# Optimization experiments

Hardware: AMD Instinct MI355X
Metric: run time of the kernel (lower is better)

The kernel has to match this reference:

```python
import jax, jax.numpy as jnp
import numpy as np

N_NODES = 100000
N_EDGES = 1600000
F_IN = 128
HID = 64
N_CLS = 40


def _sage_conv(x, src, dst, Wl, bl, Wr, num_nodes):
    # PyG SAGEConv (aggr='mean', root_weight=True, normalize=False):
    # out = lin_l(mean_{j in N(i)} x_j) + lin_r(x_i)
    msg = x[src]                                              # [E, F] gather
    agg = jax.ops.segment_sum(msg, dst, num_segments=num_nodes)
    deg = jax.ops.segment_sum(jnp.ones_like(dst, dtype=x.dtype), dst,
                              num_segments=num_nodes)
    mean = agg / jnp.maximum(deg, 1.0)[:, None]               # [N, F]
    return mean @ Wl.T + bl + x @ Wr.T


def setup_inputs() -> dict:
    key = jax.random.key(0)
    ks = jax.random.split(key, 16)

    def lin(k, out_d, in_d):
        bound = 1.0 / np.sqrt(in_d)
        return jax.random.uniform(k, (out_d, in_d), jnp.float32, -bound, bound)

    x = jax.random.normal(ks[0], (N_NODES, F_IN), jnp.float32)
    edge_index = jax.random.randint(ks[1], (2, N_EDGES), 0, N_NODES, jnp.int64)

    return {
        "x": x,
        "edge_index": edge_index,
        "W1l": lin(ks[2], HID, F_IN), "b1": jnp.zeros((HID,), jnp.float32),
        "W1r": lin(ks[3], HID, F_IN),
        "W2l": lin(ks[4], HID, HID), "b2": jnp.zeros((HID,), jnp.float32),
        "W2r": lin(ks[5], HID, HID),
        "W3l": lin(ks[6], HID, HID), "b3": jnp.zeros((HID,), jnp.float32),
        "W3r": lin(ks[7], HID, HID),
        "Wout": lin(ks[8], N_CLS, HID),
        "bout": jnp.zeros((N_CLS,), jnp.float32),
    }


def reference(x, edge_index, W1l, b1, W1r, W2l, b2, W2r, W3l, b3, W3r, Wout, bout):
    src, dst = edge_index[0], edge_index[1]
    n = x.shape[0]
    h = _sage_conv(x, src, dst, W1l, b1, W1r, n)
    h = jax.nn.elu(h)
    h = _sage_conv(h, src, dst, W2l, b2, W2r, n)
    h = jax.nn.elu(h)
    h = _sage_conv(h, src, dst, W3l, b3, W3r, n)
    return h @ Wout.T + bout
```

## Files before the change

### kernel.cpp

```cpp
#include <hip/hip_runtime.h>


static inline size_t ws_align(size_t x) { return (x + 511) & ~size_t(511); }

#define MAXBC  104
#define CAPL   96
#define EB_CAP 24576

using frag_ab = __attribute__((ext_vector_type(8))) short;
using f32x4   = __attribute__((ext_vector_type(4))) float;
using us4     = __attribute__((ext_vector_type(4))) unsigned short;

__device__ inline short f2bf(float f) {
    unsigned u = __builtin_bit_cast(unsigned, f);
    u += 0x7fff + ((u >> 16) & 1);
    return (short)(u >> 16);
}
__device__ inline float b2f(unsigned short h) {
    unsigned u = ((unsigned)h) << 16;
    return __builtin_bit_cast(float, u);
}


__global__ void zero_kernel(int* __restrict__ p, int n) {
    int i = blockIdx.x * blockDim.x + threadIdx.x;
    if (i < n) p[i] = 0;
}

__global__ void prep_all(const float* __restrict__ W1l, const float* __restrict__ W1r,
                         const float* __restrict__ W2l, const float* __restrict__ W2r,
                         const float* __restrict__ W3l, const float* __restrict__ W3r,
                         unsigned short* __restrict__ fw) {
    const int idx = blockIdx.x * 256 + threadIdx.x;
    if (idx >= 32768) return;
    const float* W;
    unsigned short* out;
    int F, rel;
    if (idx < 8192)       { W = W1l; out = fw;        F = 128; rel = idx; }
    else if (idx < 16384) { W = W1r; out = fw + 8192; F = 128; rel = idx - 8192; }
    else {
        const int q = (idx - 16384) >> 12;
        rel = (idx - 16384) & 4095;
        F = 64;
        W = (q == 0) ? W2l : (q == 1) ? W2r : (q == 2) ? W3l : W3r;
        out = fw + 16384 + q * 4096;
    }
    const int k = rel % F;
    const int col = rel / F;
    out[(k >> 3) * 512 + col * 8 + (k & 7)] = (unsigned short)f2bf(W[rel]);
}


__global__ void pass1_bin(const int* __restrict__ src, const int* __restrict__ dst,
                          int* __restrict__ bcur, unsigned* __restrict__ ebuf,
                          int nE, int nN, int nbc) {
    __shared__ unsigned lbuf[MAXBC][CAPL];
    __shared__ int bcnt[MAXBC];
    __shared__ int gbase[MAXBC];
    const int t = threadIdx.x;
    const int e0 = blockIdx.x * 4096;
    for (int i = t; i < MAXBC; i += 256) bcnt[i] = 0;
    __syncthreads();
#pragma unroll
    for (int q = 0; q < 16; ++q) {
        const int e = e0 + q * 256 + t;
        if (e < nE) {
            const unsigned d = (unsigned)dst[e];
            const unsigned s = (unsigned)src[e];
            if (d < (unsigned)nN && s < (unsigned)nN) {
                const int cb = (int)(d >> 10);
                const unsigned v = ((d & 1023u) << 17) | s;
                const int pos = atomicAdd(&bcnt[cb], 1);
                if (pos < CAPL) {
                    lbuf[cb][pos] = v;
                } else {
                    const int gp = atomicAdd(&bcur[cb], 1);
                    if (gp < EB_CAP) ebuf[(size_t)cb * EB_CAP + gp] = v;
                }
            }
        }
    }
    __syncthreads();
    for (int b = t; b < nbc; b += 256) {
        const int cnt = min(bcnt[b], CAPL);
        bcnt[b] = cnt;
        gbase[b] = (cnt > 0) ? atomicAdd(&bcur[b], cnt) : 0;
    }
    __syncthreads();
    const int wid = t >> 6, lane = t & 63;
    for (int b = wid; b < nbc; b += 4) {
        const int cnt = bcnt[b];
        const int gb = gbase[b];
        for (int i = lane; i < cnt; i += 64) {
            const int gp = gb + i;
            if (gp < EB_CAP) ebuf[(size_t)b * EB_CAP + gp] = lbuf[b][i];
        }
    }
}

__global__ void scan_buckets(const int* __restrict__ bcur, int* __restrict__ bbase, int nbc) {
    __shared__ int sdata[256];
    const int t = threadIdx.x;
    const int v = (t < nbc) ? min(bcur[t], EB_CAP) : 0;
    sdata[t] = v;
    __syncthreads();
    for (int off = 1; off < 256; off <<= 1) {
        int add = (t >= off) ? sdata[t - off] : 0;
        __syncthreads();
        sdata[t] += add;
        __syncthreads();
    }
    if (t < nbc) bbase[t] = sdata[t] - v;
}

__global__ void pass2_build(const unsigned* __restrict__ ebuf,
                            const int* __restrict__ bcur, const int* __restrict__ bbase,
                            int* __restrict__ rowptr, int* __restrict__ csr,
                            int nN, int nbc) {
    __shared__ int lcnt[1024];
    __shared__ int lcur[1024];
    __shared__ int sdata[256];
    const int b = blockIdx.x;
    const int node0 = b << 10;
    const int nloc = min(1024, nN - node0);
    if (nloc <= 0) return;
    const int cnt  = min(bcur[b], EB_CAP);
    const int base = bbase[b];
    const int t = threadIdx.x;
    const unsigned* eb = ebuf + (size_t)b * EB_CAP;

    for (int i = t; i < 1024; i += 256) lcnt[i] = 0;
    __syncthreads();
    for (int i = t; i < cnt; i += 256) atomicAdd(&lcnt[eb[i] >> 17], 1);
    __syncthreads();
    int v[4];
    int tsum = 0;
#pragma unroll
    for (int q = 0; q < 4; ++q) { v[q] = lcnt[t * 4 + q]; tsum += v[q]; }
    sdata[t] = tsum;
    __syncthreads();
    for (int off = 1; off < 256; off <<= 1) {
        int add = (t >= off) ? sdata[t - off] : 0;
        __syncthreads();
        sdata[t] += add;
        __syncthreads();
    }
    int run = sdata[t] - tsum;
#pragma unroll
    for (int q = 0; q < 4; ++q) {
        const int l = t * 4 + q;
        lcur[l] = run;
        if (l < nloc) rowptr[node0 + l] = base + run;
        run += v[q];
    }
    if (b == nbc - 1 && t == 0) rowptr[nN] = base + cnt;
    __syncthreads();
    for (int i = t; i < cnt; i += 256) {
        const unsigned ev = eb[i];
        const int pos = atomicAdd(&lcur[ev >> 17], 1);
        csr[base + pos] = (int)((ev & 0x1FFFFu) << 7);
    }
}

template<int F, bool AF32>
__global__ void proj2_mfma(const void* __restrict__ Aptr,
                           const unsigned short* __restrict__ fwl,
                           const unsigned short* __restrict__ fwr,
                           const float* __restrict__ bias,
                           unsigned short* __restrict__ xl,
                           float* __restrict__ xr,
                           int nN) {
    const int t    = threadIdx.x;
    const int wave = t >> 6;
    const int lane = t & 63;
    const int lg   = lane >> 4;
    const int lr   = lane & 15;
    const int row0 = blockIdx.x * 64 + wave * 16;

    const float*          Af = (const float*)Aptr;
    const unsigned short* Ab = (const unsigned short*)Aptr;

    f32x4 accl[4] = {};
    f32x4 accr[4] = {};

#pragma unroll
    for (int ks = 0; ks < F / 32; ++ks) {
        const int k0 = ks * 32 + lg * 8;
        frag_ab afr;
        {
            int row = row0 + lr;
            if (row >= nN) row = nN - 1;
            if constexpr (AF32) {
                const float4 f0 = *reinterpret_cast<const float4*>(Af + (size_t)row * F + k0);
                const float4 f1 = *reinterpret_cast<const float4*>(Af + (size_t)row * F + k0 + 4);
                afr[0] = f2bf(f0.x); afr[1] = f2bf(f0.y); afr[2] = f2bf(f0.z); afr[3] = f2bf(f0.w);
                afr[4] = f2bf(f1.x); afr[5] = f2bf(f1.y); afr[6] = f2bf(f1.z); afr[7] = f2bf(f1.w);
            } else {
                afr = *reinterpret_cast<const frag_ab*>(Ab + (size_t)row * F + k0);
            }
        }
        const int ob = (ks * 4 + lg) * 512;
#pragma unroll
        for (int nf = 0; nf < 4; ++nf) {
            const int col = nf * 16 + lr;
            const frag_ab bl = *reinterpret_cast<const frag_ab*>(fwl + ob + col * 8);
            const frag_ab br = *reinterpret_cast<const frag_ab*>(fwr + ob + col * 8);
            accl[nf] = __builtin_amdgcn_mfma_f32_16x16x32_bf16(afr, bl, accl[nf], 0, 0, 0);
            accr[nf] = __builtin_amdgcn_mfma_f32_16x16x32_bf16(afr, br, accr[nf], 0, 0, 0);
        }
    }

#pragma unroll
    for (int nf = 0; nf < 4; ++nf) {
        const int col = nf * 16 + lr;
        const float bv = bias[col];
#pragma unroll
        for (int j = 0; j < 4; ++j) {
            const int row = row0 + lg * 4 + j;
            if (row < nN) {
                xl[(size_t)row * 64 + col] = (unsigned short)f2bf(accl[nf][j]);
                xr[(size_t)row * 64 + col] = accr[nf][j] + bv;
            }
        }
    }
}

template<bool DOELU>
__global__ void gather_kernel(const unsigned short* __restrict__ xl,
                              const float* __restrict__ xr,
                              const int* __restrict__ rowptr, const int* __restrict__ csr,
                              unsigned short* __restrict__ outp, int nN, int nE) {
    const int node = blockIdx.x * (blockDim.x >> 6) + (threadIdx.x >> 6);
    if (node >= nN) return;
    const int lane = threadIdx.x & 63;
    int b = rowptr[node];
    int e = rowptr[node + 1];
    b = max(0, min(b, nE));
    e = max(b, min(e, nE));
    b = __builtin_amdgcn_readfirstlane(b);
    e = __builtin_amdgcn_readfirstlane(e);
    const float d = (float)(e - b);
    const char* xlb = (const char*)xl + (lane << 1);

    float acc = 0.f;
    int i = b;
    for (; i + 16 <= e; i += 16) {
        unsigned short v[16];
#pragma unroll
        for (int j = 0; j < 16; ++j) {
            const unsigned s = (unsigned)csr[i + j];
            v[j] = *(const unsigned short*)(xlb + s);
        }
#pragma unroll
        for (int j = 0; j < 16; ++j) acc += b2f(v[j]);
    }
    if (i < e) {
        const int lim = e - i;
        unsigned short v[16];
#pragma unroll
        for (int j = 0; j < 16; ++j) {
            const unsigned s = (unsigned)csr[i + min(j, lim - 1)];
            v[j] = *(const unsigned short*)(xlb + s);
        }
#pragma unroll
        for (int j = 0; j < 16; ++j) acc += (j < lim) ? b2f(v[j]) : 0.f;
    }

    float vout = acc / fmaxf(d, 1.0f) + xr[(size_t)node * 64 + lane];
    if (DOELU) vout = vout > 0.f ? vout : expm1f(vout);
    outp[(size_t)node * 64 + lane] = (unsigned short)f2bf(vout);
}

template<int F, int NOUT>
__global__ void head_kernel(const unsigned short* __restrict__ A,
                            const float* __restrict__ W,
                            const float* __restrict__ bias,
                            float* __restrict__ out, int nN) {
    constexpr int NCH = F / 32;
    __shared__ float As[64][36];
    __shared__ float Bs[32][64];

    const int t = threadIdx.x;
    const int block0 = blockIdx.x * 64;
    const int tm = (t >> 4) << 2;
    const int tn = (t & 15) << 2;

    float acc[4][4] = {};

    for (int ch = 0; ch < NCH; ++ch) {
        const int kg0 = ch * 32;
        {
            const int kk = (t & 7) * 4;
#pragma unroll
            for (int r = 0; r < 2; ++r) {
                const int n = (t >> 3) + r * 32;
                const int node = block0 + n;
                float4 v = make_float4(0.f, 0.f, 0.f, 0.f);
                if (node < nN) {
                    const us4 u = *reinterpret_cast<const us4*>(A + (size_t)node * F + kg0 + kk);
                    v.x = b2f(u[0]); v.y = b2f(u[1]); v.z = b2f(u[2]); v.w = b2f(u[3]);
                }
                *reinterpret_cast<float4*>(&As[n][kk]) = v;
            }
        }
        {
            const int j = t & 63;
#pragma unroll
            for (int p = 0; p < 8; ++p) {
                const int kk = (t >> 6) + p * 4;
                Bs[kk][j] = (j < NOUT) ? W[(size_t)j * F + kg0 + kk] : 0.0f;
            }
        }
        __syncthreads();
#pragma unroll
        for (int kk = 0; kk < 32; ++kk) {
            const float a0 = As[tm + 0][kk];
            const float a1 = As[tm + 1][kk];
            const float a2 = As[tm + 2][kk];
            const float a3 = As[tm + 3][kk];
            const float4 bv = *reinterpret_cast<const float4*>(&Bs[kk][tn]);
            acc[0][0] += a0 * bv.x; acc[0][1] += a0 * bv.y; acc[0][2] += a0 * bv.z; acc[0][3] += a0 * bv.w;
            acc[1][0] += a1 * bv.x; acc[1][1] += a1 * bv.y; acc[1][2] += a1 * bv.z; acc[1][3] += a1 * bv.w;
            acc[2][0] += a2 * bv.x; acc[2][1] += a2 * bv.y; acc[2][2] += a2 * bv.z; acc[2][3] += a2 * bv.w;
            acc[3][0] += a3 * bv.x; acc[3][1] += a3 * bv.y; acc[3][2] += a3 * bv.z; acc[3][3] += a3 * bv.w;
        }
        __syncthreads();
    }

#pragma unroll
    for (int i = 0; i < 4; ++i) {
        const int node = block0 + tm + i;
        if (node >= nN) continue;
#pragma unroll
        for (int j = 0; j < 4; ++j) {
            const int col = tn + j;
            if (col < NOUT)
                out[(size_t)node * NOUT + col] = acc[i][j] + bias[col];
        }
    }
}


extern "C" void kernel_launch(void* const* d_in, const int* in_sizes, int n_in,
                              void* d_out, int out_size, void* d_ws, size_t ws_size,
                              hipStream_t stream) {
    const float* x    = (const float*)d_in[0];
    const int*   ei   = (const int*)d_in[1];
    const float* W1l  = (const float*)d_in[2];
    const float* b1   = (const float*)d_in[3];
    const float* W1r  = (const float*)d_in[4];
    const float* W2l  = (const float*)d_in[5];
    const float* b2   = (const float*)d_in[6];
    const float* W2r  = (const float*)d_in[7];
    const float* W3l  = (const float*)d_in[8];
    const float* b3   = (const float*)d_in[9];
    const float* W3r  = (const float*)d_in[10];
    const float* Wout = (const float*)d_in[11];
    const float* bout = (const float*)d_in[12];

    const int N = in_sizes[0] / 128;
    const int E = in_sizes[1] / 2;
    const int* src  = ei;
    const int* dstA = ei + E;
    const int nbc = (N + 1023) >> 10;

    char* ws = (char*)d_ws;
    size_t o = 0;
    int* bcur    = (int*)(ws + o); o += ws_align((size_t)MAXBC * 4);
    int* bbase   = (int*)(ws + o); o += ws_align((size_t)MAXBC * 4);
    int* rowptr  = (int*)(ws + o); o += ws_align((size_t)(N + 1) * 4);
    int* csr     = (int*)(ws + o); o += ws_align((size_t)E * 4);
    unsigned* ebuf = (unsigned*)(ws + o); o += ws_align((size_t)MAXBC * EB_CAP * 4);
    unsigned short* fw  = (unsigned short*)(ws + o); o += ws_align((size_t)32768 * 2);
    unsigned short* xl  = (unsigned short*)(ws + o); o += ws_align((size_t)N * 64 * 2);
    float*          xr  = (float*)(ws + o);          o += ws_align((size_t)N * 64 * 4);
    unsigned short* hAb = (unsigned short*)(ws + o); o += ws_align((size_t)N * 64 * 2);
    unsigned short* hBb = (unsigned short*)(ws + o); o += ws_align((size_t)N * 64 * 2);
    unsigned short* h3b = (unsigned short*)(ws + o); o += ws_align((size_t)N * 64 * 2);
    float* outp = (float*)d_out;

    const int projGrid = (N + 63) / 64;
    const int gatherGrid = (N + 3) / 4;
    const int headGrid = (N + 63) / 64;

    zero_kernel<<<1, 256, 0, stream>>>(bcur, MAXBC);
    prep_all<<<128, 256, 0, stream>>>(W1l, W1r, W2l, W2r, W3l, W3r, fw);
    pass1_bin<<<(E + 4095) / 4096, 256, 0, stream>>>(src, dstA, bcur, ebuf, E, N, nbc);
    scan_buckets<<<1, 256, 0, stream>>>(bcur, bbase, nbc);
    pass2_build<<<nbc, 256, 0, stream>>>(ebuf, bcur, bbase, rowptr, csr, N, nbc);

    const unsigned short* fw1l = fw;
    const unsigned short* fw1r = fw + 8192;
    const unsigned short* fw2l = fw + 16384;
    const unsigned short* fw2r = fw + 16384 + 4096;
    const unsigned short* fw3l = fw + 16384 + 8192;
    const unsigned short* fw3r = fw + 16384 + 12288;

    proj2_mfma<128, true><<<projGrid, 256, 0, stream>>>(x, fw1l, fw1r, b1, xl, xr, N);
    gather_kernel<true><<<gatherGrid, 256, 0, stream>>>(xl, xr, rowptr, csr, hAb, N, E);

    proj2_mfma<64, false><<<projGrid, 256, 0, stream>>>(hAb, fw2l, fw2r, b2, xl, xr, N);
    gather_kernel<true><<<gatherGrid, 256, 0, stream>>>(xl, xr, rowptr, csr, hBb, N, E);

    proj2_mfma<64, false><<<projGrid, 256, 0, stream>>>(hBb, fw3l, fw3r, b3, xl, xr, N);
    gather_kernel<false><<<gatherGrid, 256, 0, stream>>>(xl, xr, rowptr, csr, h3b, N, E);

    head_kernel<64, 40><<<headGrid, 256, 0, stream>>>(h3b, Wout, bout, outp, N);
}
```

Baseline: 274.5 us.

## Store root projection in bf16 and gather two nodes per wave

The root-term projection xr is now written and read as bf16 instead of fp32, halving its write and read traffic. The gather kernel also has each wave process two destination nodes at once, interleaving their neighbor loads so more independent gathers are in flight. The grid is halved to match. This adds bf16 rounding to the root term, and the paired loop adds branching plus imbalance when the two nodes have different degrees.

```diff
diff --git a/kernel.cpp b/kernel.cpp
--- a/kernel.cpp
+++ b/kernel.cpp
@@ -168,7 +168,7 @@
                            const unsigned short* __restrict__ fwr,
                            const float* __restrict__ bias,
                            unsigned short* __restrict__ xl,
-                           float* __restrict__ xr,
+                           unsigned short* __restrict__ xr,
                            int nN) {
     const int t    = threadIdx.x;
     const int wave = t >> 6;
@@ -219,7 +219,7 @@
             const int row = row0 + lg * 4 + j;
             if (row < nN) {
                 xl[(size_t)row * 64 + col] = (unsigned short)f2bf(accl[nf][j]);
-                xr[(size_t)row * 64 + col] = accr[nf][j] + bv;
+                xr[(size_t)row * 64 + col] = (unsigned short)f2bf(accr[nf][j] + bv);
             }
         }
     }
@@ -227,48 +227,74 @@
 
 template<bool DOELU>
 __global__ void gather_kernel(const unsigned short* __restrict__ xl,
-                              const float* __restrict__ xr,
+                              const unsigned short* __restrict__ xr,
                               const int* __restrict__ rowptr, const int* __restrict__ csr,
                               unsigned short* __restrict__ outp, int nN, int nE) {
-    const int node = blockIdx.x * (blockDim.x >> 6) + (threadIdx.x >> 6);
-    if (node >= nN) return;
+    const int waveId = blockIdx.x * 4 + ((threadIdx.x >> 6));
+    const int nA = waveId * 2;
+    const int nB = nA + 1;
+    if (nA >= nN) return;
     const int lane = threadIdx.x & 63;
-    int b = rowptr[node];
-    int e = rowptr[node + 1];
-    b = max(0, min(b, nE));
-    e = max(b, min(e, nE));
-    b = __builtin_amdgcn_readfirstlane(b);
-    e = __builtin_amdgcn_readfirstlane(e);
-    const float d = (float)(e - b);
     const char* xlb = (const char*)xl + (lane << 1);
 
-    float acc = 0.f;
-    int i = b;
-    for (; i + 16 <= e; i += 16) {
-        unsigned short v[16];
-#pragma unroll
-        for (int j = 0; j < 16; ++j) {
-            const unsigned s = (unsigned)csr[i + j];
-            v[j] = *(const unsigned short*)(xlb + s);
-        }
-#pragma unroll
-        for (int j = 0; j < 16; ++j) acc += b2f(v[j]);
-    }
-    if (i < e) {
-        const int lim = e - i;
-        unsigned short v[16];
-#pragma unroll
-        for (int j = 0; j < 16; ++j) {
-            const unsigned s = (unsigned)csr[i + min(j, lim - 1)];
-            v[j] = *(const unsigned short*)(xlb + s);
-        }
-#pragma unroll
-        for (int j = 0; j < 16; ++j) acc += (j < lim) ? b2f(v[j]) : 0.f;
-    }
-
-    float vout = acc / fmaxf(d, 1.0f) + xr[(size_t)node * 64 + lane];
-    if (DOELU) vout = vout > 0.f ? vout : expm1f(vout);
-    outp[(size_t)node * 64 + lane] = (unsigned short)f2bf(vout);
+    int bA = rowptr[nA];
+    int eA = rowptr[nA + 1];
+    bA = max(0, min(bA, nE)); eA = max(bA, min(eA, nE));
+    bA = __builtin_amdgcn_readfirstlane(bA);
+    eA = __builtin_amdgcn_readfirstlane(eA);
+    int bB = 0, eB = 0;
+    if (nB < nN) {
+        bB = rowptr[nB];
+        eB = rowptr[nB + 1];
+        bB = max(0, min(bB, nE)); eB = max(bB, min(eB, nE));
+        bB = __builtin_amdgcn_readfirstlane(bB);
+        eB = __builtin_amdgcn_readfirstlane(eB);
+    }
+    const float dA = (float)(eA - bA);
+    const float dB = (float)(eB - bB);
+
+    float accA = 0.f, accB = 0.f;
+    int iA = bA, iB = bB;
+    while (iA < eA || iB < eB) {
+        const int limA = min(eA - iA, 16);
+        const int limB = min(eB - iB, 16);
+        unsigned short vA[16], vB[16];
+        if (limA > 0) {
+#pragma unroll
+            for (int j = 0; j < 16; ++j) {
+                const unsigned s = (unsigned)csr[iA + min(j, limA - 1)];
+                vA[j] = *(const unsigned short*)(xlb + s);
+            }
+        }
+        if (limB > 0) {
+#pragma unroll
+            for (int j = 0; j < 16; ++j) {
+                const unsigned s = (unsigned)csr[iB + min(j, limB - 1)];
+                vB[j] = *(const unsigned short*)(xlb + s);
+            }
+        }
+        if (limA > 0) {
+#pragma unroll
+            for (int j = 0; j < 16; ++j) accA += (j < limA) ? b2f(vA[j]) : 0.f;
+            iA += limA;
+        }
+        if (limB > 0) {
+#pragma unroll
+            for (int j = 0; j < 16; ++j) accB += (j < limB) ? b2f(vB[j]) : 0.f;
+            iB += limB;
+        }
+    }
+
+    {
+        float v = accA / fmaxf(dA, 1.0f) + b2f(xr[(size_t)nA * 64 + lane]);
+        if (DOELU) v = v > 0.f ? v : expm1f(v);
+        outp[(size_t)nA * 64 + lane] = (unsigned short)f2bf(v);
+    }
+    if (nB < nN) {
+        float v = accB / fmaxf(dB, 1.0f) + b2f(xr[(size_t)nB * 64 + lane]);
+        if (DOELU) v = v > 0.f ? v : expm1f(v);
+        outp[(size_t)nB * 64 + lane] = (unsigned short)f2bf(v);
+    }
 }
 
 template<int F, int NOUT>
@@ -373,14 +399,14 @@
     unsigned* ebuf = (unsigned*)(ws + o); o += ws_align((size_t)MAXBC * EB_CAP * 4);
     unsigned short* fw  = (unsigned short*)(ws + o); o += ws_align((size_t)32768 * 2);
     unsigned short* xl  = (unsigned short*)(ws + o); o += ws_align((size_t)N * 64 * 2);
-    float*          xr  = (float*)(ws + o);          o += ws_align((size_t)N * 64 * 4);
+    unsigned short* xr  = (unsigned short*)(ws + o); o += ws_align((size_t)N * 64 * 2);
     unsigned short* hAb = (unsigned short*)(ws + o); o += ws_align((size_t)N * 64 * 2);
     unsigned short* hBb = (unsigned short*)(ws + o); o += ws_align((size_t)N * 64 * 2);
     unsigned short* h3b = (unsigned short*)(ws + o); o += ws_align((size_t)N * 64 * 2);
     float* outp = (float*)d_out;
 
     const int projGrid = (N + 63) / 64;
-    const int gatherGrid = (N + 3) / 4;
+    const int gatherGrid = (N + 7) / 8;
     const int headGrid = (N + 63) / 64;
 
     zero_kernel<<<1, 256, 0, stream>>>(bcur, MAXBC);
```

Measured after the change: 386.9 us. +40.9%, slower.
